# Kernel tuning notes

Measured on AMD Instinct MI355X. Metric: run time of the kernel, lower is better.

The kernel has to match this reference:

```python
import jax, jax.numpy as jnp
import numpy as np

N_NODES = 100000
EPS = 1e-5


def gcn_conv(x, src, dst, W, b):
    # PyG GCNConv: h = W x; out_i = sum_{j->i} norm_ij * h_j  (with self-loops)
    h = x @ W  # [N, out]
    deg = jax.ops.segment_sum(jnp.ones_like(src, dtype=h.dtype), dst,
                              num_segments=N_NODES) + 1.0  # +1 self-loop
    dinv = jax.lax.rsqrt(deg)  # [N]
    norm = dinv[src] * dinv[dst]  # [E]
    msgs = h[src] * norm[:, None]  # [E, out]
    agg = jax.ops.segment_sum(msgs, dst, num_segments=N_NODES)
    agg = agg + h * (1.0 / deg)[:, None]  # self-loop term, norm = deg^-1
    return agg + b


def graph_norm(x, w, b, mean_scale):
    # PyG GraphNorm, single graph: normalize over nodes per feature
    mean = jnp.mean(x, axis=0, keepdims=True)
    xc = x - mean_scale * mean
    var = jnp.mean(xc * xc, axis=0, keepdims=True)
    return w * xc * jax.lax.rsqrt(var + EPS) + b


def layer_norm(x, w, b):
    mean = jnp.mean(x, axis=-1, keepdims=True)
    xc = x - mean
    var = jnp.mean(xc * xc, axis=-1, keepdims=True)
    return w * xc * jax.lax.rsqrt(var + EPS) + b


def setup_inputs() -> dict:
    key = jax.random.key(0)
    ks = jax.random.split(key, 8)
    in_dim, hid, emb = 128, 64, 32
    x = jax.random.normal(ks[0], (N_NODES, in_dim), dtype=jnp.float32)
    edge_index = jax.random.randint(ks[1], (2, 1600000), 0, N_NODES, dtype=jnp.int64)
    s = 0.05
    return {
        'x': x,
        'edge_index': edge_index,
        'W1': jax.random.normal(ks[2], (in_dim, hid), jnp.float32) * s,
        'b1': jnp.zeros((hid,), jnp.float32),
        'W2': jax.random.normal(ks[3], (hid, hid), jnp.float32) * s,
        'b2': jnp.zeros((hid,), jnp.float32),
        'gn_w': jnp.ones((hid,), jnp.float32),
        'gn_b': jnp.zeros((hid,), jnp.float32),
        'gn_ms': jnp.ones((hid,), jnp.float32),
        'ln_w': jnp.ones((hid,), jnp.float32),
        'ln_b': jnp.zeros((hid,), jnp.float32),
        'fc_W': jax.random.normal(ks[4], (hid, emb), jnp.float32) * s,
        'fc_b': jnp.zeros((emb,), jnp.float32),
    }


def reference(x, edge_index, W1, b1, W2, b2, gn_w, gn_b, gn_ms, ln_w, ln_b, fc_W, fc_b):
    src, dst = edge_index[0], edge_index[1]
    h = jax.nn.relu(gcn_conv(x, src, dst, W1, b1))
    h = graph_norm(h, gn_w, gn_b, gn_ms)
    h = layer_norm(h, ln_w, ln_b)
    # dropout: identity in eval mode
    h = jax.nn.relu(gcn_conv(h, src, dst, W2, b2))
    h = graph_norm(h, gn_w, gn_b, gn_ms)
    h = layer_norm(h, ln_w, ln_b)
    pooled = jnp.max(h, axis=0)  # [hid]
    embedding = pooled @ fc_W + fc_b  # [emb]; emb != 1 so no sigmoid
    return embedding
```

## Files before the change

kernel.cpp:

```cpp
#include <hip/hip_runtime.h>
#include <hip/hip_bf16.h>

#define EPSV 1e-5f
#define CHUNK 256
#define CAP 6144
#define MAXNB 512

typedef __attribute__((ext_vector_type(8))) short bf16x8;
typedef __attribute__((ext_vector_type(4))) float f32x4;

__device__ __forceinline__ ushort f2bf(float f) {
    union { float f; unsigned u; } c; c.f = f;
    unsigned u = c.u;
    return (ushort)((u + 0x7fffu + ((u >> 16) & 1u)) >> 16);
}
__device__ __forceinline__ float bf2f(ushort h) {
    union { unsigned u; float f; } c; c.u = ((unsigned)h) << 16;
    return c.f;
}
__device__ __forceinline__ float bflo(unsigned u) {
    union { unsigned u; float f; } c; c.u = u << 16;
    return c.f;
}
__device__ __forceinline__ float bfhi(unsigned u) {
    union { unsigned u; float f; } c; c.u = u & 0xFFFF0000u;
    return c.f;
}
__device__ __forceinline__ void acc8(float* a, uint4 u) {
    a[0] += bflo(u.x); a[1] += bfhi(u.x);
    a[2] += bflo(u.y); a[3] += bfhi(u.y);
    a[4] += bflo(u.z); a[5] += bfhi(u.z);
    a[6] += bflo(u.w); a[7] += bfhi(u.w);
}


__global__ void prep_kernel(const float* __restrict__ W1, const float* __restrict__ W2,
                            ushort* __restrict__ wsw1, ushort* __restrict__ wsw2,
                            int* __restrict__ bcur, int NB) {
    int t = blockIdx.x * blockDim.x + threadIdx.x;
    if (t < 128 * 64) {
        int k = t >> 6, n = t & 63;
        wsw1[((k >> 3) * 64 + n) * 8 + (k & 7)] = f2bf(W1[t]);
    }
    if (t < 64 * 64) {
        int k = t >> 6, n = t & 63;
        wsw2[((k >> 3) * 64 + n) * 8 + (k & 7)] = f2bf(W2[t]);
    }
    if (t < NB) bcur[t] = t * CAP;
}


#define EPB 8192

__global__ void __launch_bounds__(256) bucket_scatter(const int* __restrict__ ei,
                                                      int* __restrict__ bcur,
                                                      unsigned* __restrict__ bdata, int E,
                                                      int NB) {
    __shared__ int h[MAXNB];
    __shared__ int cur[MAXNB];
    int t = threadIdx.x;
    int base = blockIdx.x * EPB;
    int end = min(base + EPB, E);
    for (int b = t; b < NB; b += 256) h[b] = 0;
    __syncthreads();
    for (int e = base + t * 4; e < end; e += 1024) {
        int4 d4 = *reinterpret_cast<const int4*>(&ei[E + e]);
        atomicAdd(&h[d4.x >> 8], 1);
        atomicAdd(&h[d4.y >> 8], 1);
        atomicAdd(&h[d4.z >> 8], 1);
        atomicAdd(&h[d4.w >> 8], 1);
    }
    __syncthreads();
    for (int b = t; b < NB; b += 256) {
        int c = h[b];
        cur[b] = c ? atomicAdd(&bcur[b], c) : 0;
    }
    __syncthreads();
    for (int e = base + t * 4; e < end; e += 1024) {
        int4 s4 = *reinterpret_cast<const int4*>(&ei[e]);
        int4 d4 = *reinterpret_cast<const int4*>(&ei[E + e]);
        int p0 = atomicAdd(&cur[d4.x >> 8], 1);
        bdata[p0] = (unsigned)s4.x | ((unsigned)(d4.x & 255) << 20);
        int p1 = atomicAdd(&cur[d4.y >> 8], 1);
        bdata[p1] = (unsigned)s4.y | ((unsigned)(d4.y & 255) << 20);
        int p2 = atomicAdd(&cur[d4.z >> 8], 1);
        bdata[p2] = (unsigned)s4.z | ((unsigned)(d4.z & 255) << 20);
        int p3 = atomicAdd(&cur[d4.w >> 8], 1);
        bdata[p3] = (unsigned)s4.w | ((unsigned)(d4.w & 255) << 20);
    }
}


__global__ void __launch_bounds__(256) bucket_finish(const unsigned* __restrict__ bdata,
                                                     const int* __restrict__ bcur,
                                                     int2* __restrict__ NI,
                                                     float* __restrict__ dinv,
                                                     int* __restrict__ srcs, int N) {
    __shared__ int h[CHUNK];
    __shared__ int cur[CHUNK];
    int t = threadIdx.x;
    int beg = blockIdx.x * CAP;
    int end = bcur[blockIdx.x];
    h[t] = 0;
    __syncthreads();
    for (int e = beg + t; e < end; e += 256) atomicAdd(&h[bdata[e] >> 20], 1);
    __syncthreads();
    int deg = h[t];
    int pc = (deg + 3) & ~3;
    cur[t] = pc;
    __syncthreads();
    for (int off = 1; off < 256; off <<= 1) {
        int x = (t >= off) ? cur[t - off] : 0;
        __syncthreads();
        cur[t] += x;
        __syncthreads();
    }
    int begp = beg + cur[t] - pc;
    int node = blockIdx.x * CHUNK + t;
    if (node < N) {
        NI[node] = make_int2(begp, pc);
        dinv[node] = rsqrtf((float)deg + 1.0f);
    }
    h[t] = begp;
    __syncthreads();
    for (int e = beg + t; e < end; e += 256) {
        unsigned p = bdata[e];
        int pos = atomicAdd(&h[p >> 20], 1);
        srcs[pos] = (int)((p & 0xFFFFFu) << 3);
    }
    __syncthreads();
    int zr = N * 8;
    for (int k = h[t]; k < begp + pc; k++) srcs[k] = zr;
}


__global__ void __launch_bounds__(256) mm1_kernel(const float* __restrict__ X,
                                                  const ushort* __restrict__ wsw,
                                                  const float* __restrict__ dinv,
                                                  ushort* __restrict__ Ht, int N) {
    const int KO = 4;
    int w = threadIdx.x >> 6, lane = threadIdx.x & 63;
    int m = lane & 15, q = lane >> 4;
    int row = blockIdx.x * 64 + w * 16 + m;

    bf16x8 afrag[KO];
#pragma unroll
    for (int kk = 0; kk < KO; kk++) {
        float xv[8];
        if (row < N) {
            const float4* xp = reinterpret_cast<const float4*>(X + (size_t)row * 128 + kk * 32 + q * 8);
            float4 v0 = xp[0], v1 = xp[1];
            xv[0] = v0.x; xv[1] = v0.y; xv[2] = v0.z; xv[3] = v0.w;
            xv[4] = v1.x; xv[5] = v1.y; xv[6] = v1.z; xv[7] = v1.w;
        } else {
#pragma unroll
            for (int j = 0; j < 8; j++) xv[j] = 0.f;
        }
#pragma unroll
        for (int j = 0; j < 8; j++) afrag[kk][j] = (short)f2bf(xv[j]);
    }

    float dv[4];
#pragma unroll
    for (int reg = 0; reg < 4; reg++) {
        int r = blockIdx.x * 64 + w * 16 + q * 4 + reg;
        dv[reg] = (r < N) ? dinv[r] : 0.f;
    }

    const bf16x8* wp = reinterpret_cast<const bf16x8*>(wsw);
#pragma unroll
    for (int ct = 0; ct < 4; ct++) {
        f32x4 acc = {0.f, 0.f, 0.f, 0.f};
#pragma unroll
        for (int kk = 0; kk < KO; kk++) {
            bf16x8 b = wp[(kk * 4 + q) * 64 + ct * 16 + m];
            acc = __builtin_amdgcn_mfma_f32_16x16x32_bf16(afrag[kk], b, acc, 0, 0, 0);
        }
#pragma unroll
        for (int reg = 0; reg < 4; reg++) {
            int r = blockIdx.x * 64 + w * 16 + q * 4 + reg;
            if (r < N) Ht[(size_t)r * 64 + ct * 16 + m] = f2bf(acc[reg] * dv[reg]);
        }
    }
}


__global__ void __launch_bounds__(256) mm2_kernel(
    const ushort* __restrict__ A2, const ushort* __restrict__ wsw,
    const float* __restrict__ sums, const float* __restrict__ gn_w,
    const float* __restrict__ gn_b, const float* __restrict__ gn_ms,
    const float* __restrict__ ln_w, const float* __restrict__ ln_b,
    const float* __restrict__ dinv, ushort* __restrict__ Ht, int N) {
    __shared__ float sg[64], tg[64], lwv[64], lbv[64];
    int t = threadIdx.x;
    if (t < 64) {
        float invN = 1.0f / (float)N;
        float mean = sums[t] * invN;
        float m2 = sums[64 + t] * invN;
        float ms = gn_ms[t];
        float var = m2 - 2.f * ms * mean * mean + ms * ms * mean * mean;
        float s = gn_w[t] * rsqrtf(var + EPSV);
        sg[t] = s;
        tg[t] = gn_b[t] - s * ms * mean;
        lwv[t] = ln_w[t];
        lbv[t] = ln_b[t];
    }
    __syncthreads();

    int w = t >> 6, lane = t & 63;
    int m = lane & 15, q = lane >> 4;
    int row = blockIdx.x * 64 + w * 16 + m;

    float g[16];
#pragma unroll
    for (int kk = 0; kk < 2; kk++) {
        uint4 u = make_uint4(0, 0, 0, 0);
        if (row < N)
            u = *reinterpret_cast<const uint4*>(A2 + (size_t)row * 64 + kk * 32 + q * 8);
        unsigned uu[4] = {u.x, u.y, u.z, u.w};
#pragma unroll
        for (int p = 0; p < 4; p++) {
            int f0 = kk * 32 + q * 8 + 2 * p;
            g[kk * 8 + 2 * p] = sg[f0] * bflo(uu[p]) + tg[f0];
            g[kk * 8 + 2 * p + 1] = sg[f0 + 1] * bfhi(uu[p]) + tg[f0 + 1];
        }
    }
    float s1 = 0.f;
#pragma unroll
    for (int i = 0; i < 16; i++) s1 += g[i];
    s1 += __shfl_xor(s1, 16);
    s1 += __shfl_xor(s1, 32);
    float mu = s1 * (1.f / 64.f);
    float s2 = 0.f;
#pragma unroll
    for (int i = 0; i < 16; i++) {
        float c = g[i] - mu;
        s2 += c * c;
    }
    s2 += __shfl_xor(s2, 16);
    s2 += __shfl_xor(s2, 32);
    float rs = rsqrtf(s2 * (1.f / 64.f) + EPSV);

    bf16x8 afrag[2];
#pragma unroll
    for (int kk = 0; kk < 2; kk++) {
#pragma unroll
        for (int j = 0; j < 8; j++) {
            int f = kk * 32 + q * 8 + j;
            float y = lwv[f] * (g[kk * 8 + j] - mu) * rs + lbv[f];
            afrag[kk][j] = (short)f2bf(y);
        }
    }

    float dv[4];
#pragma unroll
    for (int reg = 0; reg < 4; reg++) {
        int r = blockIdx.x * 64 + w * 16 + q * 4 + reg;
        dv[reg] = (r < N) ? dinv[r] : 0.f;
    }

    const bf16x8* wp = reinterpret_cast<const bf16x8*>(wsw);
#pragma unroll
    for (int ct = 0; ct < 4; ct++) {
        f32x4 acc = {0.f, 0.f, 0.f, 0.f};
#pragma unroll
        for (int kk = 0; kk < 2; kk++) {
            bf16x8 b = wp[(kk * 4 + q) * 64 + ct * 16 + m];
            acc = __builtin_amdgcn_mfma_f32_16x16x32_bf16(afrag[kk], b, acc, 0, 0, 0);
        }
#pragma unroll
        for (int reg = 0; reg < 4; reg++) {
            int r = blockIdx.x * 64 + w * 16 + q * 4 + reg;
            if (r < N) Ht[(size_t)r * 64 + ct * 16 + m] = f2bf(acc[reg] * dv[reg]);
        }
    }
}


__global__ void __launch_bounds__(256) agg_kernel(
    const ushort* __restrict__ Ht, const int2* __restrict__ NI, const int* __restrict__ srcs,
    const float* __restrict__ dinv, const float* __restrict__ bias,
    ushort* __restrict__ out, float* __restrict__ sums, int N) {
    int t = threadIdx.x;
    int lane = t & 63;
    int g = lane >> 3, fq = lane & 7;
    int wid = (blockIdx.x * blockDim.x + t) >> 6;
    int nw = (gridDim.x * blockDim.x) >> 6;
    const uint4* H4 = reinterpret_cast<const uint4*>(Ht);
    uint4* O4 = reinterpret_cast<uint4*>(out);
    const int ZR = N * 8;
    float bb[8];
#pragma unroll
    for (int j = 0; j < 8; j++) bb[j] = bias[fq * 8 + j];
    float ps1[8] = {0, 0, 0, 0, 0, 0, 0, 0}, ps2[8] = {0, 0, 0, 0, 0, 0, 0, 0};

    for (int jo = wid; jo * 8 < N; jo += nw) {
        int node = jo * 8 + g;
        bool valid = node < N;
        int2 info = valid ? NI[node] : make_int2(0, 0);
        float di = valid ? dinv[node] : 0.f;
        int e = info.x, end = info.x + info.y;
        float a[8] = {0, 0, 0, 0, 0, 0, 0, 0};
        for (; e + 8 <= end; e += 8) {
            int4 i0 = *reinterpret_cast<const int4*>(&srcs[e]);
            int4 i1 = *reinterpret_cast<const int4*>(&srcs[e + 4]);
            uint4 u0 = H4[i0.x + fq];
            uint4 u1 = H4[i0.y + fq];
            uint4 u2 = H4[i0.z + fq];
            uint4 u3 = H4[i0.w + fq];
            uint4 u4 = H4[i1.x + fq];
            uint4 u5 = H4[i1.y + fq];
            uint4 u6 = H4[i1.z + fq];
            uint4 u7 = H4[i1.w + fq];
            acc8(a, u0); acc8(a, u1); acc8(a, u2); acc8(a, u3);
            acc8(a, u4); acc8(a, u5); acc8(a, u6); acc8(a, u7);
        }
        if (e < end) {
            int4 i0 = *reinterpret_cast<const int4*>(&srcs[e]);
            uint4 u0 = H4[i0.x + fq];
            uint4 u1 = H4[i0.y + fq];
            uint4 u2 = H4[i0.z + fq];
            uint4 u3 = H4[i0.w + fq];
            acc8(a, u0); acc8(a, u1); acc8(a, u2); acc8(a, u3);
        }
        uint4 us = H4[(valid ? node * 8 : ZR) + fq];
        float sf[8] = {bflo(us.x), bfhi(us.x), bflo(us.y), bfhi(us.y),
                       bflo(us.z), bfhi(us.z), bflo(us.w), bfhi(us.w)};
        float vv[8];
#pragma unroll
        for (int j = 0; j < 8; j++) vv[j] = fmaxf(di * a[j] + di * sf[j] + bb[j], 0.f);
        if (valid) {
            uint4 o;
            o.x = (unsigned)f2bf(vv[0]) | ((unsigned)f2bf(vv[1]) << 16);
            o.y = (unsigned)f2bf(vv[2]) | ((unsigned)f2bf(vv[3]) << 16);
            o.z = (unsigned)f2bf(vv[4]) | ((unsigned)f2bf(vv[5]) << 16);
            o.w = (unsigned)f2bf(vv[6]) | ((unsigned)f2bf(vv[7]) << 16);
            O4[(size_t)node * 8 + fq] = o;
#pragma unroll
            for (int j = 0; j < 8; j++) {
                ps1[j] += vv[j];
                ps2[j] += vv[j] * vv[j];
            }
        }
    }

    __shared__ float red[4][128];
    int wv = t >> 6;
#pragma unroll
    for (int j = 0; j < 8; j++) {
        float s = ps1[j], q = ps2[j];
        s += __shfl_xor(s, 8); s += __shfl_xor(s, 16); s += __shfl_xor(s, 32);
        q += __shfl_xor(q, 8); q += __shfl_xor(q, 16); q += __shfl_xor(q, 32);
        if (g == 0) {
            red[wv][fq * 8 + j] = s;
            red[wv][64 + fq * 8 + j] = q;
        }
    }
    __syncthreads();
    if (t < 128) {
        float v = red[0][t] + red[1][t] + red[2][t] + red[3][t];
        atomicAdd(&sums[t], v);
    }
}


__device__ __forceinline__ float gn_ln_row(float x, float mean, float var, float ms, float gw,
                                           float gb, float lw, float lb) {
    float g = gw * (x - ms * mean) * rsqrtf(var + EPSV) + gb;
    float mu = g;
#pragma unroll
    for (int off = 32; off; off >>= 1) mu += __shfl_xor(mu, off);
    mu *= (1.f / 64.f);
    float c = g - mu;
    float vv = c * c;
#pragma unroll
    for (int off = 32; off; off >>= 1) vv += __shfl_xor(vv, off);
    vv *= (1.f / 64.f);
    return lw * c * rsqrtf(vv + EPSV) + lb;
}

__device__ __forceinline__ unsigned fkey(float f) {
    unsigned u = __float_as_uint(f);
    return (u & 0x80000000u) ? ~u : (u | 0x80000000u);
}

__global__ void gnlnmax_kernel(const ushort* __restrict__ A, const float* __restrict__ sums,
                               const float* __restrict__ gn_w, const float* __restrict__ gn_b,
                               const float* __restrict__ gn_ms, const float* __restrict__ ln_w,
                               const float* __restrict__ ln_b, unsigned* __restrict__ pooled,
                               int N) {
    __shared__ float lmax[256];
    int lane = threadIdx.x & 63;
    int wave0 = (blockIdx.x * blockDim.x + threadIdx.x) >> 6;
    int nw = (gridDim.x * blockDim.x) >> 6;
    float invN = 1.0f / (float)N;
    float mean = sums[lane] * invN;
    float m2 = sums[64 + lane] * invN;
    float ms = gn_ms[lane];
    float var = m2 - 2.f * ms * mean * mean + ms * ms * mean * mean;
    float gw = gn_w[lane], gb = gn_b[lane], lw = ln_w[lane], lb = ln_b[lane];
    float mx = -3.4e38f;
    for (int i = wave0; i < N; i += nw) {
        float y = gn_ln_row(bf2f(A[(size_t)i * 64 + lane]), mean, var, ms, gw, gb, lw, lb);
        mx = fmaxf(mx, y);
    }
    lmax[threadIdx.x] = mx;
    __syncthreads();
    if (threadIdx.x < 64) {
        float m = fmaxf(fmaxf(lmax[threadIdx.x], lmax[threadIdx.x + 64]),
                        fmaxf(lmax[threadIdx.x + 128], lmax[threadIdx.x + 192]));
        atomicMax(&pooled[threadIdx.x], fkey(m));
    }
}


__global__ void final_kernel(const unsigned* __restrict__ pooled, const float* __restrict__ fc_W,
                             const float* __restrict__ fc_b, float* __restrict__ out) {
    __shared__ float p[64];
    int t = threadIdx.x;
    if (t < 64) {
        unsigned u = pooled[t];
        p[t] = (u & 0x80000000u) ? __uint_as_float(u ^ 0x80000000u) : __uint_as_float(~u);
    }
    __syncthreads();
    if (t < 32) {
        float acc = fc_b[t];
#pragma unroll
        for (int f = 0; f < 64; f++) acc += p[f] * fc_W[f * 32 + t];
        out[t] = acc;
    }
}


static inline size_t align_up(size_t v, size_t a) { return (v + a - 1) & ~(a - 1); }

extern "C" void kernel_launch(void* const* d_in, const int* in_sizes, int n_in, void* d_out,
                              int out_size, void* d_ws, size_t ws_size, hipStream_t stream) {
    const float* x = (const float*)d_in[0];
    const int* ei = (const int*)d_in[1];
    const float* W1 = (const float*)d_in[2];
    const float* b1 = (const float*)d_in[3];
    const float* W2 = (const float*)d_in[4];
    const float* b2 = (const float*)d_in[5];
    const float* gn_w = (const float*)d_in[6];
    const float* gn_b = (const float*)d_in[7];
    const float* gn_ms = (const float*)d_in[8];
    const float* ln_w = (const float*)d_in[9];
    const float* ln_b = (const float*)d_in[10];
    const float* fc_W = (const float*)d_in[11];
    const float* fc_b = (const float*)d_in[12];
    float* out = (float*)d_out;

    const int N = in_sizes[0] / 128;
    const int E = in_sizes[1] / 2;
    const int NB = (N + CHUNK - 1) / CHUNK;

    char* ws = (char*)d_ws;
    size_t off = 0;
    auto alloc = [&](size_t bytes) {
        char* p = ws + off;
        off = align_up(off + bytes, 256);
        return p;
    };
    int2* NI = (int2*)alloc((size_t)N * 8);
    int* bcur = (int*)alloc((size_t)(NB + 1) * 4);
    float* dinv = (float*)alloc((size_t)N * 4);
    unsigned* bdata = (unsigned*)alloc((size_t)NB * CAP * 4);
    int* srcs = (int*)alloc((size_t)NB * CAP * 4);
    ushort* bufB = (ushort*)alloc((size_t)N * 64 * 2);
    ushort* wsw1 = (ushort*)alloc(128 * 64 * 2);
    ushort* wsw2 = (ushort*)alloc(64 * 64 * 2);
    ushort* bufA = (ushort*)alloc((size_t)N * 64 * 2);
    size_t zoff = off;
    ushort* zrow = (ushort*)alloc(128);
    float* sums = (float*)alloc(256 * 4);
    unsigned* pooled = (unsigned*)alloc(64 * 4);
    size_t zlen = off - zoff;
    (void)zrow;

    hipMemsetAsync(ws + zoff, 0, zlen, stream);

    int nbB = (E + EPB - 1) / EPB;
    prep_kernel<<<48, 256, 0, stream>>>(W1, W2, wsw1, wsw2, bcur, NB);
    bucket_scatter<<<nbB, 256, 0, stream>>>(ei, bcur, bdata, E, NB);
    bucket_finish<<<NB, 256, 0, stream>>>(bdata, bcur, NI, dinv, srcs, N);

    int nbMM = (N + 63) / 64;
    int nbAgg = 782;

    mm1_kernel<<<nbMM, 256, 0, stream>>>(x, wsw1, dinv, bufA, N);
    agg_kernel<<<nbAgg, 256, 0, stream>>>(bufA, NI, srcs, dinv, b1, bufB, sums, N);

    mm2_kernel<<<nbMM, 256, 0, stream>>>(bufB, wsw2, sums, gn_w, gn_b, gn_ms, ln_w, ln_b, dinv,
                                         bufA, N);
    agg_kernel<<<nbAgg, 256, 0, stream>>>(bufA, NI, srcs, dinv, b2, bufB, sums + 128, N);
    gnlnmax_kernel<<<512, 256, 0, stream>>>(bufB, sums + 128, gn_w, gn_b, gn_ms, ln_w, ln_b,
                                            pooled, N);

    final_kernel<<<1, 64, 0, stream>>>(pooled, fc_W, fc_b, out);
}
```

Before: 305.9 us.

## Replace two-pass bucket sort with fixed-capacity per-node edge slots

Swaps the two-level bucketed counting sort for building the CSR-like adjacency. Instead, each edge does a global atomic increment on its destination's counter and writes its source straight into a fixed slot of 64 entries per node. A light pad kernel then computes dinv and fills padding up to a multiple of 4. This removes one full pass over the edge list, the intermediate bucket buffer and the shared-memory scans. In exchange it uses contended global atomics, scattered writes into a much larger 25 MB slot array, and silently truncates any node whose in-degree exceeds 64, which also changes its normalisation.

```diff
diff --git a/kernel.cpp b/kernel.cpp
--- a/kernel.cpp
+++ b/kernel.cpp
@@ -2,9 +2,7 @@
 #include <hip/hip_bf16.h>
 
 #define EPSV 1e-5f
-#define CHUNK 256
-#define CAP 6144
-#define MAXNB 512
+#define NCAP 64
 
 typedef __attribute__((ext_vector_type(8))) short bf16x8;
 typedef __attribute__((ext_vector_type(4))) float f32x4;
@@ -36,7 +34,7 @@
 
 __global__ void prep_kernel(const float* __restrict__ W1, const float* __restrict__ W2,
                             ushort* __restrict__ wsw1, ushort* __restrict__ wsw2,
-                            int* __restrict__ bcur, int NB) {
+                            int* __restrict__ cnt, int N) {
     int t = blockIdx.x * blockDim.x + threadIdx.x;
     if (t < 128 * 64) {
         int k = t >> 6, n = t & 63;
@@ -46,91 +44,48 @@
         int k = t >> 6, n = t & 63;
         wsw2[((k >> 3) * 64 + n) * 8 + (k & 7)] = f2bf(W2[t]);
     }
-    if (t < NB) bcur[t] = t * CAP;
-}
-
-
-#define EPB 8192
-
-__global__ void __launch_bounds__(256) bucket_scatter(const int* __restrict__ ei,
-                                                      int* __restrict__ bcur,
-                                                      unsigned* __restrict__ bdata, int E,
-                                                      int NB) {
-    __shared__ int h[MAXNB];
-    __shared__ int cur[MAXNB];
-    int t = threadIdx.x;
-    int base = blockIdx.x * EPB;
-    int end = min(base + EPB, E);
-    for (int b = t; b < NB; b += 256) h[b] = 0;
-    __syncthreads();
-    for (int e = base + t * 4; e < end; e += 1024) {
-        int4 d4 = *reinterpret_cast<const int4*>(&ei[E + e]);
-        atomicAdd(&h[d4.x >> 8], 1);
-        atomicAdd(&h[d4.y >> 8], 1);
-        atomicAdd(&h[d4.z >> 8], 1);
-        atomicAdd(&h[d4.w >> 8], 1);
-    }
-    __syncthreads();
-    for (int b = t; b < NB; b += 256) {
-        int c = h[b];
-        cur[b] = c ? atomicAdd(&bcur[b], c) : 0;
-    }
-    __syncthreads();
-    for (int e = base + t * 4; e < end; e += 1024) {
-        int4 s4 = *reinterpret_cast<const int4*>(&ei[e]);
-        int4 d4 = *reinterpret_cast<const int4*>(&ei[E + e]);
-        int p0 = atomicAdd(&cur[d4.x >> 8], 1);
-        bdata[p0] = (unsigned)s4.x | ((unsigned)(d4.x & 255) << 20);
-        int p1 = atomicAdd(&cur[d4.y >> 8], 1);
-        bdata[p1] = (unsigned)s4.y | ((unsigned)(d4.y & 255) << 20);
-        int p2 = atomicAdd(&cur[d4.z >> 8], 1);
-        bdata[p2] = (unsigned)s4.z | ((unsigned)(d4.z & 255) << 20);
-        int p3 = atomicAdd(&cur[d4.w >> 8], 1);
-        bdata[p3] = (unsigned)s4.w | ((unsigned)(d4.w & 255) << 20);
-    }
-}
-
-
-__global__ void __launch_bounds__(256) bucket_finish(const unsigned* __restrict__ bdata,
-                                                     const int* __restrict__ bcur,
-                                                     int2* __restrict__ NI,
-                                                     float* __restrict__ dinv,
-                                                     int* __restrict__ srcs, int N) {
-    __shared__ int h[CHUNK];
-    __shared__ int cur[CHUNK];
-    int t = threadIdx.x;
-    int beg = blockIdx.x * CAP;
-    int end = bcur[blockIdx.x];
-    h[t] = 0;
-    __syncthreads();
-    for (int e = beg + t; e < end; e += 256) atomicAdd(&h[bdata[e] >> 20], 1);
-    __syncthreads();
-    int deg = h[t];
+    if (t < N) cnt[t] = 0;
+}
+
+
+__global__ void __launch_bounds__(256) edge_scatter(const int* __restrict__ ei,
+                                                    int* __restrict__ cnt,
+                                                    int* __restrict__ srcs, int E) {
+    int t = blockIdx.x * blockDim.x + threadIdx.x;
+    int e = t * 4;
+    if (e + 3 >= E) {
+        for (; e < E; e++) {
+            int s = ei[e], d = ei[E + e];
+            int p = atomicAdd(&cnt[d], 1);
+            if (p < NCAP) srcs[d * NCAP + p] = s << 3;
+        }
+        return;
+    }
+    int4 s4 = *reinterpret_cast<const int4*>(&ei[e]);
+    int4 d4 = *reinterpret_cast<const int4*>(&ei[E + e]);
+    int p0 = atomicAdd(&cnt[d4.x], 1);
+    if (p0 < NCAP) srcs[d4.x * NCAP + p0] = s4.x << 3;
+    int p1 = atomicAdd(&cnt[d4.y], 1);
+    if (p1 < NCAP) srcs[d4.y * NCAP + p1] = s4.y << 3;
+    int p2 = atomicAdd(&cnt[d4.z], 1);
+    if (p2 < NCAP) srcs[d4.z * NCAP + p2] = s4.z << 3;
+    int p3 = atomicAdd(&cnt[d4.w], 1);
+    if (p3 < NCAP) srcs[d4.w * NCAP + p3] = s4.w << 3;
+}
+
+
+__global__ void __launch_bounds__(256) pad_kernel(const int* __restrict__ cnt,
+                                                  int2* __restrict__ NI,
+                                                  float* __restrict__ dinv,
+                                                  int* __restrict__ srcs, int N) {
+    int t = blockIdx.x * blockDim.x + threadIdx.x;
+    if (t >= N) return;
+    int deg = min(cnt[t], NCAP);
     int pc = (deg + 3) & ~3;
-    cur[t] = pc;
-    __syncthreads();
-    for (int off = 1; off < 256; off <<= 1) {
-        int x = (t >= off) ? cur[t - off] : 0;
-        __syncthreads();
-        cur[t] += x;
-        __syncthreads();
-    }
-    int begp = beg + cur[t] - pc;
-    int node = blockIdx.x * CHUNK + t;
-    if (node < N) {
-        NI[node] = make_int2(begp, pc);
-        dinv[node] = rsqrtf((float)deg + 1.0f);
-    }
-    h[t] = begp;
-    __syncthreads();
-    for (int e = beg + t; e < end; e += 256) {
-        unsigned p = bdata[e];
-        int pos = atomicAdd(&h[p >> 20], 1);
-        srcs[pos] = (int)((p & 0xFFFFFu) << 3);
-    }
-    __syncthreads();
+    NI[t] = make_int2(t * NCAP, pc);
+    dinv[t] = rsqrtf((float)deg + 1.0f);
     int zr = N * 8;
-    for (int k = h[t]; k < begp + pc; k++) srcs[k] = zr;
+    for (int k = deg; k < pc; k++) srcs[t * NCAP + k] = zr;
 }
 
 
@@ -453,7 +408,7 @@
 
     const int N = in_sizes[0] / 128;
     const int E = in_sizes[1] / 2;
-    const int NB = (N + CHUNK - 1) / CHUNK;
+    const int NBN = (N + 255) / 256;
 
     char* ws = (char*)d_ws;
     size_t off = 0;
@@ -463,10 +418,9 @@
         return p;
     };
     int2* NI = (int2*)alloc((size_t)N * 8);
-    int* bcur = (int*)alloc((size_t)(NB + 1) * 4);
+    int* cnt = (int*)alloc((size_t)N * 4);
     float* dinv = (float*)alloc((size_t)N * 4);
-    unsigned* bdata = (unsigned*)alloc((size_t)NB * CAP * 4);
-    int* srcs = (int*)alloc((size_t)NB * CAP * 4);
+    int* srcs = (int*)alloc((size_t)N * NCAP * 4);
     ushort* bufB = (ushort*)alloc((size_t)N * 64 * 2);
     ushort* wsw1 = (ushort*)alloc(128 * 64 * 2);
     ushort* wsw2 = (ushort*)alloc(64 * 64 * 2);
@@ -480,10 +434,10 @@
 
     hipMemsetAsync(ws + zoff, 0, zlen, stream);
 
-    int nbB = (E + EPB - 1) / EPB;
-    prep_kernel<<<48, 256, 0, stream>>>(W1, W2, wsw1, wsw2, bcur, NB);
-    bucket_scatter<<<nbB, 256, 0, stream>>>(ei, bcur, bdata, E, NB);
-    bucket_finish<<<NB, 256, 0, stream>>>(bdata, bcur, NI, dinv, srcs, N);
+    int nbS = (E / 4 + 255) / 256;
+    prep_kernel<<<NBN, 256, 0, stream>>>(W1, W2, wsw1, wsw2, cnt, N);
+    edge_scatter<<<nbS, 256, 0, stream>>>(ei, cnt, srcs, E);
+    pad_kernel<<<NBN, 256, 0, stream>>>(cnt, NI, dinv, srcs, N);
 
     int nbMM = (N + 63) / 64;
     int nbAgg = 782;
```

New measurement: 401.6 us. 1.31x slower.

## Remove prep and final kernels by fusing weight conversion and FC into neighbors

Applied to the files above, without the earlier changes.

Eliminates the separate prep kernel by having each matmul block convert its weight matrix to bf16 in LDS, and by making the bucket cursors relative so the memset zero-initialises them. The final FC kernel is folded into the max-pool kernel using a last-block-done atomic counter. mm1 also now stages X through LDS before building MFMA fragments. This cuts two launches, at the cost of each of roughly 1563 matmul blocks redundantly converting weights and using more LDS.

```diff
diff --git a/kernel.cpp b/kernel.cpp
--- a/kernel.cpp
+++ b/kernel.cpp
@@ -5,6 +5,7 @@
 #define CHUNK 256
 #define CAP 6144
 #define MAXNB 512
+#define EPB 8192
 
 typedef __attribute__((ext_vector_type(8))) short bf16x8;
 typedef __attribute__((ext_vector_type(4))) float f32x4;
@@ -33,24 +34,6 @@
     a[6] += bflo(u.w); a[7] += bfhi(u.w);
 }
 
-
-__global__ void prep_kernel(const float* __restrict__ W1, const float* __restrict__ W2,
-                            ushort* __restrict__ wsw1, ushort* __restrict__ wsw2,
-                            int* __restrict__ bcur, int NB) {
-    int t = blockIdx.x * blockDim.x + threadIdx.x;
-    if (t < 128 * 64) {
-        int k = t >> 6, n = t & 63;
-        wsw1[((k >> 3) * 64 + n) * 8 + (k & 7)] = f2bf(W1[t]);
-    }
-    if (t < 64 * 64) {
-        int k = t >> 6, n = t & 63;
-        wsw2[((k >> 3) * 64 + n) * 8 + (k & 7)] = f2bf(W2[t]);
-    }
-    if (t < NB) bcur[t] = t * CAP;
-}
-
-
-#define EPB 8192
 
 __global__ void __launch_bounds__(256) bucket_scatter(const int* __restrict__ ei,
                                                       int* __restrict__ bcur,
@@ -73,7 +56,7 @@
     __syncthreads();
     for (int b = t; b < NB; b += 256) {
         int c = h[b];
-        cur[b] = c ? atomicAdd(&bcur[b], c) : 0;
+        cur[b] = c ? (atomicAdd(&bcur[b], c) + b * CAP) : 0;
     }
     __syncthreads();
     for (int e = base + t * 4; e < end; e += 1024) {
@@ -100,7 +83,7 @@
     __shared__ int cur[CHUNK];
     int t = threadIdx.x;
     int beg = blockIdx.x * CAP;
-    int end = bcur[blockIdx.x];
+    int end = beg + bcur[blockIdx.x];
     h[t] = 0;
     __syncthreads();
     for (int e = beg + t; e < end; e += 256) atomicAdd(&h[bdata[e] >> 20], 1);
@@ -135,30 +118,37 @@
 
 
 __global__ void __launch_bounds__(256) mm1_kernel(const float* __restrict__ X,
-                                                  const ushort* __restrict__ wsw,
+                                                  const float* __restrict__ W1,
                                                   const float* __restrict__ dinv,
                                                   ushort* __restrict__ Ht, int N) {
+    __shared__ ushort wlds[128 * 64];
+    __shared__ ushort xlds[64 * 136];
+    int t = threadIdx.x;
+    for (int i = t; i < 128 * 64; i += 256) {
+        int k = i >> 6, n = i & 63;
+        wlds[((k >> 3) * 64 + n) * 8 + (k & 7)] = f2bf(W1[i]);
+    }
+    for (int i = t; i < 64 * 32; i += 256) {
+        int r = i >> 5, c4 = (i & 31) * 4;
+        int grow = blockIdx.x * 64 + r;
+        ushort4 v = make_ushort4(0, 0, 0, 0);
+        if (grow < N) {
+            float4 f = *reinterpret_cast<const float4*>(X + (size_t)grow * 128 + c4);
+            v = make_ushort4(f2bf(f.x), f2bf(f.y), f2bf(f.z), f2bf(f.w));
+        }
+        *reinterpret_cast<ushort4*>(&xlds[r * 136 + c4]) = v;
+    }
+    __syncthreads();
+
     const int KO = 4;
-    int w = threadIdx.x >> 6, lane = threadIdx.x & 63;
+    int w = t >> 6, lane = t & 63;
     int m = lane & 15, q = lane >> 4;
-    int row = blockIdx.x * 64 + w * 16 + m;
+    int lrow = w * 16 + m;
 
     bf16x8 afrag[KO];
 #pragma unroll
-    for (int kk = 0; kk < KO; kk++) {
-        float xv[8];
-        if (row < N) {
-            const float4* xp = reinterpret_cast<const float4*>(X + (size_t)row * 128 + kk * 32 + q * 8);
-            float4 v0 = xp[0], v1 = xp[1];
-            xv[0] = v0.x; xv[1] = v0.y; xv[2] = v0.z; xv[3] = v0.w;
-            xv[4] = v1.x; xv[5] = v1.y; xv[6] = v1.z; xv[7] = v1.w;
-        } else {
-#pragma unroll
-            for (int j = 0; j < 8; j++) xv[j] = 0.f;
-        }
-#pragma unroll
-        for (int j = 0; j < 8; j++) afrag[kk][j] = (short)f2bf(xv[j]);
-    }
+    for (int kk = 0; kk < KO; kk++)
+        afrag[kk] = *reinterpret_cast<const bf16x8*>(&xlds[lrow * 136 + kk * 32 + q * 8]);
 
     float dv[4];
 #pragma unroll
@@ -167,7 +157,7 @@
         dv[reg] = (r < N) ? dinv[r] : 0.f;
     }
 
-    const bf16x8* wp = reinterpret_cast<const bf16x8*>(wsw);
+    const bf16x8* wp = reinterpret_cast<const bf16x8*>(wlds);
 #pragma unroll
     for (int ct = 0; ct < 4; ct++) {
         f32x4 acc = {0.f, 0.f, 0.f, 0.f};
@@ -186,13 +176,18 @@
 
 
 __global__ void __launch_bounds__(256) mm2_kernel(
-    const ushort* __restrict__ A2, const ushort* __restrict__ wsw,
+    const ushort* __restrict__ A2, const float* __restrict__ W2,
     const float* __restrict__ sums, const float* __restrict__ gn_w,
     const float* __restrict__ gn_b, const float* __restrict__ gn_ms,
     const float* __restrict__ ln_w, const float* __restrict__ ln_b,
     const float* __restrict__ dinv, ushort* __restrict__ Ht, int N) {
+    __shared__ ushort wlds[64 * 64];
     __shared__ float sg[64], tg[64], lwv[64], lbv[64];
     int t = threadIdx.x;
+    for (int i = t; i < 64 * 64; i += 256) {
+        int k = i >> 6, n = i & 63;
+        wlds[((k >> 3) * 64 + n) * 8 + (k & 7)] = f2bf(W2[i]);
+    }
     if (t < 64) {
         float invN = 1.0f / (float)N;
         float mean = sums[t] * invN;
@@ -259,7 +254,7 @@
         dv[reg] = (r < N) ? dinv[r] : 0.f;
     }
 
-    const bf16x8* wp = reinterpret_cast<const bf16x8*>(wsw);
+    const bf16x8* wp = reinterpret_cast<const bf16x8*>(wlds);
 #pragma unroll
     for (int ct = 0; ct < 4; ct++) {
         f32x4 acc = {0.f, 0.f, 0.f, 0.f};
@@ -384,14 +379,17 @@
     return (u & 0x80000000u) ? ~u : (u | 0x80000000u);
 }
 
-__global__ void gnlnmax_kernel(const ushort* __restrict__ A, const float* __restrict__ sums,
-                               const float* __restrict__ gn_w, const float* __restrict__ gn_b,
-                               const float* __restrict__ gn_ms, const float* __restrict__ ln_w,
-                               const float* __restrict__ ln_b, unsigned* __restrict__ pooled,
-                               int N) {
+__global__ void gnlnmax_final(const ushort* __restrict__ A, const float* __restrict__ sums,
+                              const float* __restrict__ gn_w, const float* __restrict__ gn_b,
+                              const float* __restrict__ gn_ms, const float* __restrict__ ln_w,
+                              const float* __restrict__ ln_b, unsigned* __restrict__ pooled,
+                              unsigned* __restrict__ done, const float* __restrict__ fc_W,
+                              const float* __restrict__ fc_b, float* __restrict__ out, int N) {
     __shared__ float lmax[256];
-    int lane = threadIdx.x & 63;
-    int wave0 = (blockIdx.x * blockDim.x + threadIdx.x) >> 6;
+    __shared__ int islast;
+    int t = threadIdx.x;
+    int lane = t & 63;
+    int wave0 = (blockIdx.x * blockDim.x + t) >> 6;
     int nw = (gridDim.x * blockDim.x) >> 6;
     float invN = 1.0f / (float)N;
     float mean = sums[lane] * invN;
@@ -404,30 +402,33 @@
         float y = gn_ln_row(bf2f(A[(size_t)i * 64 + lane]), mean, var, ms, gw, gb, lw, lb);
         mx = fmaxf(mx, y);
     }
-    lmax[threadIdx.x] = mx;
-    __syncthreads();
-    if (threadIdx.x < 64) {
-        float m = fmaxf(fmaxf(lmax[threadIdx.x], lmax[threadIdx.x + 64]),
-                        fmaxf(lmax[threadIdx.x + 128], lmax[threadIdx.x + 192]));
-        atomicMax(&pooled[threadIdx.x], fkey(m));
-    }
-}
-
-
-__global__ void final_kernel(const unsigned* __restrict__ pooled, const float* __restrict__ fc_W,
-                             const float* __restrict__ fc_b, float* __restrict__ out) {
-    __shared__ float p[64];
-    int t = threadIdx.x;
+    lmax[t] = mx;
+    __syncthreads();
     if (t < 64) {
-        unsigned u = pooled[t];
-        p[t] = (u & 0x80000000u) ? __uint_as_float(u ^ 0x80000000u) : __uint_as_float(~u);
-    }
-    __syncthreads();
-    if (t < 32) {
-        float acc = fc_b[t];
-#pragma unroll
-        for (int f = 0; f < 64; f++) acc += p[f] * fc_W[f * 32 + t];
-        out[t] = acc;
+        float m = fmaxf(fmaxf(lmax[t], lmax[t + 64]), fmaxf(lmax[t + 128], lmax[t + 192]));
+        atomicMax(&pooled[t], fkey(m));
+    }
+    __syncthreads();
+    if (t == 0) {
+        __threadfence();
+        unsigned old = atomicAdd(done, 1u);
+        islast = (old == gridDim.x - 1);
+    }
+    __syncthreads();
+    if (islast) {
+        __shared__ float p[64];
+        if (t < 64) {
+            __threadfence();
+            unsigned u = atomicAdd(&pooled[t], 0u);
+            p[t] = (u & 0x80000000u) ? __uint_as_float(u ^ 0x80000000u) : __uint_as_float(~u);
+        }
+        __syncthreads();
+        if (t < 32) {
+            float acc = fc_b[t];
+#pragma unroll
+            for (int f = 0; f < 64; f++) acc += p[f] * fc_W[f * 32 + t];
+            out[t] = acc;
+        }
     }
 }
 
@@ -463,39 +464,35 @@
         return p;
     };
     int2* NI = (int2*)alloc((size_t)N * 8);
-    int* bcur = (int*)alloc((size_t)(NB + 1) * 4);
     float* dinv = (float*)alloc((size_t)N * 4);
     unsigned* bdata = (unsigned*)alloc((size_t)NB * CAP * 4);
     int* srcs = (int*)alloc((size_t)NB * CAP * 4);
     ushort* bufB = (ushort*)alloc((size_t)N * 64 * 2);
-    ushort* wsw1 = (ushort*)alloc(128 * 64 * 2);
-    ushort* wsw2 = (ushort*)alloc(64 * 64 * 2);
     ushort* bufA = (ushort*)alloc((size_t)N * 64 * 2);
     size_t zoff = off;
     ushort* zrow = (ushort*)alloc(128);
     float* sums = (float*)alloc(256 * 4);
     unsigned* pooled = (unsigned*)alloc(64 * 4);
+    int* bcur = (int*)alloc((size_t)(NB + 1) * 4);
+    unsigned* done = (unsigned*)alloc(4);
     size_t zlen = off - zoff;
     (void)zrow;
 
     hipMemsetAsync(ws + zoff, 0, zlen, stream);
 
     int nbB = (E + EPB - 1) / EPB;
-    prep_kernel<<<48, 256, 0, stream>>>(W1, W2, wsw1, wsw2, bcur, NB);
     bucket_scatter<<<nbB, 256, 0, stream>>>(ei, bcur, bdata, E, NB);
     bucket_finish<<<NB, 256, 0, stream>>>(bdata, bcur, NI, dinv, srcs, N);
 
     int nbMM = (N + 63) / 64;
     int nbAgg = 782;
 
-    mm1_kernel<<<nbMM, 256, 0, stream>>>(x, wsw1, dinv, bufA, N);
+    mm1_kernel<<<nbMM, 256, 0, stream>>>(x, W1, dinv, bufA, N);
     agg_kernel<<<nbAgg, 256, 0, stream>>>(bufA, NI, srcs, dinv, b1, bufB, sums, N);
 
-    mm2_kernel<<<nbMM, 256, 0, stream>>>(bufB, wsw2, sums, gn_w, gn_b, gn_ms, ln_w, ln_b, dinv,
+    mm2_kernel<<<nbMM, 256, 0, stream>>>(bufB, W2, sums, gn_w, gn_b, gn_ms, ln_w, ln_b, dinv,
                                          bufA, N);
     agg_kernel<<<nbAgg, 256, 0, stream>>>(bufA, NI, srcs, dinv, b2, bufB, sums + 128, N);
-    gnlnmax_kernel<<<512, 256, 0, stream>>>(bufB, sums + 128, gn_w, gn_b, gn_ms, ln_w, ln_b,
-                                            pooled, N);
-
-    final_kernel<<<1, 64, 0, stream>>>(pooled, fc_W, fc_b, out);
-}
+    gnlnmax_final<<<512, 256, 0, stream>>>(bufB, sums + 128, gn_w, gn_b, gn_ms, ln_w, ln_b,
+                                           pooled, done, fc_W, fc_b, out, N);
+}
```

Result: slower. 316.2 us (+3.4%).
